# Performance work log

Hardware: AMD Instinct MI355X
Metric: run time of the kernel (lower is better)

The kernel has to match this reference:

```python
import jax, jax.numpy as jnp
import numpy as np

LN_EPS = 1e-5

def _linear(x, w, b):
    return x @ w.T + b

def _layernorm(x, g, b):
    mu = jnp.mean(x, axis=-1, keepdims=True)
    var = jnp.var(x, axis=-1, keepdims=True)
    return (x - mu) * jax.lax.rsqrt(var + LN_EPS) * g + b

def _depthwise_conv1d(x, w):
    # x: [B, S, D], w: [D, 1, 3] (torch layout), padding=1, groups=D, no bias
    xc = jnp.swapaxes(x, 1, 2)  # [B, D, S]
    y = jax.lax.conv_general_dilated(
        xc, w, window_strides=(1,), padding=[(1, 1)],
        dimension_numbers=('NCH', 'OIH', 'NCH'),
        feature_group_count=w.shape[0])
    return jnp.swapaxes(y, 1, 2)

def _ssm(x, A, B, C):
    # h_t = h_{t-1} A^T + x_t B^T ; y_t = h_t C^T
    bsz = x.shape[0]
    h0 = jnp.zeros((bsz, A.shape[0]), dtype=x.dtype)
    def step(h, xt):  # xt: [B, D]
        h = h @ A.T + xt @ B.T
        return h, h @ C.T
    _, ys = jax.lax.scan(step, h0, jnp.swapaxes(x, 0, 1))  # [S, B, D]
    return jnp.swapaxes(ys, 0, 1)

def setup_inputs() -> dict:
    key = jax.random.key(0)
    d_model, d_state, expand = 1024, 64, 2
    B, S = 4, 2048
    ks = jax.random.split(key, 16)
    sm = 1.0 / np.sqrt(d_model)
    inp = {
        'x': jax.random.normal(ks[0], (B, S, d_model), jnp.float32),
        'w1_w': jax.random.normal(ks[1], (d_model, d_model), jnp.float32) * sm,
        'w1_b': jnp.zeros((d_model,), jnp.float32),
        'v1_w': jax.random.normal(ks[2], (d_model, d_model), jnp.float32) * sm,
        'v1_b': jnp.zeros((d_model,), jnp.float32),
        'w2_w': jax.random.normal(ks[3], (d_model, d_model), jnp.float32) * sm,
        'w2_b': jnp.zeros((d_model,), jnp.float32),
        'conv_w': jax.random.normal(ks[4], (d_model, 1, 3), jnp.float32) * (1.0 / np.sqrt(3.0)),
        'A': jax.random.normal(ks[5], (d_state, d_state), jnp.float32) * 0.05,  # spectral radius ~0.4, stable scan
        'Bm': jax.random.normal(ks[6], (d_state, d_model), jnp.float32) * sm,
        'Cm': jax.random.normal(ks[7], (d_model, d_state), jnp.float32) * (1.0 / np.sqrt(d_state)),
        'ln1_g': jnp.ones((d_model,), jnp.float32),
        'ln1_b': jnp.zeros((d_model,), jnp.float32),
        'ln2_g': jnp.ones((d_model,), jnp.float32),
        'ln2_b': jnp.zeros((d_model,), jnp.float32),
        'ff1_w': jax.random.normal(ks[8], (expand * d_model, d_model), jnp.float32) * sm,
        'ff1_b': jnp.zeros((expand * d_model,), jnp.float32),
        'ff2_w': jax.random.normal(ks[9], (d_model, expand * d_model), jnp.float32) * (1.0 / np.sqrt(expand * d_model)),
        'ff2_b': jnp.zeros((d_model,), jnp.float32),
    }
    return inp

def reference(x, w1_w, w1_b, v1_w, v1_b, w2_w, w2_b, conv_w, A, Bm, Cm,
              ln1_g, ln1_b, ln2_g, ln2_b, ff1_w, ff1_b, ff2_w, ff2_b):
    residual = x
    h = _layernorm(x, ln1_g, ln1_b)
    # Mamba block
    x1 = _linear(h, w1_w, w1_b)
    xc = jax.nn.silu(_depthwise_conv1d(x1, conv_w))
    x_ssm = _ssm(xc, A, Bm, Cm)
    v = jax.nn.silu(_linear(h, v1_w, v1_b))
    h = _linear(x_ssm * v, w2_w, w2_b)
    x = h + residual
    residual = x
    h = _layernorm(x, ln2_g, ln2_b)
    h = _linear(jax.nn.gelu(_linear(h, ff1_w, ff1_b), approximate=False), ff2_w, ff2_b)
    return h + residual
```

## Files before the change

### kernel.cpp

```cpp
#include <hip/hip_runtime.h>
#include <hip/hip_bf16.h>

typedef unsigned short u16;
typedef __bf16 bf16x8 __attribute__((ext_vector_type(8)));
typedef float f32x4 __attribute__((ext_vector_type(4)));

#define DEV __device__ __forceinline__

DEV u16 f2bf(float f) {
  __hip_bfloat16 h = __float2bfloat16(f);
  union { __hip_bfloat16 h; u16 u; } c; c.h = h; return c.u;
}
DEV float bf2f(u16 u) {
  unsigned int x = ((unsigned int)u) << 16; float f;
  __builtin_memcpy(&f, &x, 4); return f;
}
DEV float silu_f(float x) { return x / (1.f + __expf(-x)); }
DEV float gelu_f(float x) { return 0.5f * x * (1.f + erff(x * 0.70710678118654752f)); }

DEV void gl_lds16(const void* g, void* l) {
  __builtin_amdgcn_global_load_lds(
      (const __attribute__((address_space(1))) void*)g,
      (__attribute__((address_space(3))) void*)l, 16, 0, 0);
}

template<int N> DEV void vmwait() {
  static_assert(N == 0 || N == 2 || N == 4, "unsupported vmcnt");
  if constexpr (N == 0)      asm volatile("s_waitcnt vmcnt(0)" ::: "memory");
  else if constexpr (N == 2) asm volatile("s_waitcnt vmcnt(2)" ::: "memory");
  else                       asm volatile("s_waitcnt vmcnt(4)" ::: "memory");
}

template<int BM, int EPI>
__global__ __launch_bounds__(512, 2)
void gemm256(const u16* __restrict__ A, const u16* __restrict__ Bw,
             const float* __restrict__ bias, const float* __restrict__ bias2,
             const float* __restrict__ resp,
             void* __restrict__ outp, void* __restrict__ outp2,
             int M, int N, int K)
{
  constexpr int WROWS = BM / 2;
  constexpr int MR = WROWS / 16;
  constexpr int NR = 4;
  constexpr int LA = BM / 64;
  constexpr int LB = 4;
  constexpr int AE = BM * 64;
  constexpr int BUFE = AE + 16384;
  __shared__ alignas(16) u16 lds[2 * BUFE];

  const int t = threadIdx.x;
  const int w = t >> 6, l = t & 63;
  const int wm = w >> 2, wn = w & 3;
  const int lr = l & 15, lq = l >> 4;

  const int nwg = gridDim.x;
  int lin = blockIdx.x;
  if ((nwg & 7) == 0) lin = (lin & 7) * (nwg >> 3) + (lin >> 3);
  const int nbx = N >> 8;
  const int by = lin / nbx, bx = lin - by * nbx;
  const int brow = by * BM, bcol = bx << 8;

  const int ir = l >> 3, ik = l & 7;
  const int kkl = ik ^ ir;
  const u16* gsA[LA];
  const u16* gsB[LB];
#pragma unroll
  for (int s = 0; s < LA; ++s)
    gsA[s] = A + (size_t)(brow + (w * LA + s) * 8 + ir) * K + kkl * 8;
#pragma unroll
  for (int s = 0; s < LB; ++s)
    gsB[s] = Bw + (size_t)(bcol + (w * LB + s) * 8 + ir) * K + kkl * 8;

  auto stageA = [&](int buf) {
#pragma unroll
    for (int s = 0; s < LA; ++s) {
      gl_lds16(gsA[s], &lds[buf * BUFE + (w * LA + s) * 512]);
      gsA[s] += 64;
    }
  };
  auto stageB = [&](int buf) {
#pragma unroll
    for (int s = 0; s < LB; ++s) {
      gl_lds16(gsB[s], &lds[buf * BUFE + AE + (w * LB + s) * 512]);
      gsB[s] += 64;
    }
  };

  f32x4 acc[MR][NR] = {};

  auto kstep = [&](int buf, int ks) {
    bf16x8 af[MR], bfr[NR];
#pragma unroll
    for (int mi = 0; mi < MR; ++mi) {
      const int ro = wm * WROWS + mi * 16 + lr;
      const int ck = (ks * 4 + lq) ^ (ro & 7);
      af[mi] = *(const bf16x8*)&lds[buf * BUFE + ro * 64 + ck * 8];
    }
#pragma unroll
    for (int ni = 0; ni < NR; ++ni) {
      const int ro = wn * 64 + ni * 16 + lr;
      const int ck = (ks * 4 + lq) ^ (ro & 7);
      bfr[ni] = *(const bf16x8*)&lds[buf * BUFE + AE + ro * 64 + ck * 8];
    }
    __builtin_amdgcn_s_setprio(1);
#pragma unroll
    for (int mi = 0; mi < MR; ++mi)
#pragma unroll
      for (int ni = 0; ni < NR; ++ni)
        acc[mi][ni] = __builtin_amdgcn_mfma_f32_16x16x32_bf16(af[mi], bfr[ni], acc[mi][ni], 0, 0, 0);
    __builtin_amdgcn_s_setprio(0);
  };

  stageA(0); stageB(0);
  const int nt = K >> 6;
  int cur = 0;
  for (int kt = 0; kt < nt; ++kt) {
    const int nxt = cur ^ 1;
    if (kt + 1 < nt) { stageA(nxt); vmwait<LA>(); }
    else             { vmwait<0>(); }
    __builtin_amdgcn_s_barrier();
    kstep(cur, 0);
    if (kt + 1 < nt) stageB(nxt);
    kstep(cur, 1);
    __builtin_amdgcn_s_barrier();
    cur = nxt;
  }

#pragma unroll
  for (int ni = 0; ni < NR; ++ni) {
    const int col = bcol + wn * 64 + ni * 16 + lr;
    float bv = 0.f;
    if (EPI == 3 || EPI == 4) bv = bias[col];
    if (EPI == 5) bv = (col < 1024) ? bias[col] : bias2[col - 1024];
#pragma unroll
    for (int mi = 0; mi < MR; ++mi) {
      const int row0 = brow + wm * WROWS + mi * 16 + lq * 4;
#pragma unroll
      for (int r = 0; r < 4; ++r) {
        const int row = row0 + r;
        const float raw = acc[mi][ni][r];
        if (EPI == 3) {
          const size_t idx = (size_t)row * N + col;
          ((float*)outp)[idx] = raw + bv + resp[idx];
        } else if (EPI == 4) {
          ((u16*)outp)[(size_t)row * N + col] = f2bf(gelu_f(raw + bv));
        } else {
          if (col < 1024) ((u16*)outp)[(size_t)row * 1024 + col] = f2bf(raw + bv);
          else ((u16*)outp2)[(size_t)row * 1024 + (col - 1024)] = f2bf(silu_f(raw + bv));
        }
      }
    }
  }
}

template<int EPI>
__global__ __launch_bounds__(256)
void gemm_bt(const u16* __restrict__ A, const u16* __restrict__ Bw,
             const float* __restrict__ bias, const u16* __restrict__ mulp,
             void* __restrict__ outp, int M, int N, int K)
{
  __shared__ u16 As[2][128 * 32];
  __shared__ u16 Bs[2][128 * 32];
  const int t = threadIdx.x;
  const int w = t >> 6, l = t & 63;
  const int wr = w >> 1, wc = w & 1;
  const int brow = blockIdx.y << 7;
  const int bcol = blockIdx.x << 7;

  const u16* gA0 = A + (size_t)(brow + (t >> 2)) * K + ((t & 3) << 3);
  const u16* gA1 = gA0 + (size_t)64 * K;
  int bn0 = bcol + (t >> 2);      if (bn0 > N - 1) bn0 = N - 1;
  int bn1 = bcol + 64 + (t >> 2); if (bn1 > N - 1) bn1 = N - 1;
  const u16* gB0 = Bw + (size_t)bn0 * K + ((t & 3) << 3);
  const u16* gB1 = Bw + (size_t)bn1 * K + ((t & 3) << 3);
  const int woff = w << 9;

  auto stage = [&](int b) {
    gl_lds16(gA0, &As[b][woff]);        gl_lds16(gA1, &As[b][2048 + woff]);
    gl_lds16(gB0, &Bs[b][woff]);        gl_lds16(gB1, &Bs[b][2048 + woff]);
    gA0 += 32; gA1 += 32; gB0 += 32; gB1 += 32;
  };

  f32x4 acc[4][4] = {};
  const int lr = l & 15, lk = (l >> 4) << 3;
  const int nt = K >> 5;

  stage(0);
  __syncthreads();
  int cur = 0;
  for (int kt = 0; kt < nt; ++kt) {
    if (kt + 1 < nt) stage(cur ^ 1);
    bf16x8 af[4], bfr[4];
#pragma unroll
    for (int i = 0; i < 4; ++i)
      af[i] = *(const bf16x8*)&As[cur][(wr * 64 + i * 16 + lr) * 32 + lk];
#pragma unroll
    for (int j = 0; j < 4; ++j)
      bfr[j] = *(const bf16x8*)&Bs[cur][(wc * 64 + j * 16 + lr) * 32 + lk];
    __builtin_amdgcn_s_setprio(1);
#pragma unroll
    for (int i = 0; i < 4; ++i)
#pragma unroll
      for (int j = 0; j < 4; ++j)
        acc[i][j] = __builtin_amdgcn_mfma_f32_16x16x32_bf16(af[i], bfr[j], acc[i][j], 0, 0, 0);
    __builtin_amdgcn_s_setprio(0);
    __syncthreads();
    cur ^= 1;
  }

  const int lq = l >> 4;
#pragma unroll
  for (int j = 0; j < 4; ++j) {
    const int col = bcol + wc * 64 + j * 16 + lr;
    if (col >= N) continue;
    const float bv = (EPI == 0 && bias) ? bias[col] : 0.f;
#pragma unroll
    for (int i = 0; i < 4; ++i) {
      const int row0 = brow + wr * 64 + i * 16 + lq * 4;
#pragma unroll
      for (int r = 0; r < 4; ++r) {
        const size_t idx = (size_t)(row0 + r) * N + col;
        const float raw = acc[i][j][r];
        if (EPI == 0) ((float*)outp)[idx] = raw + bv;
        else          ((u16*)outp)[idx]   = f2bf(raw * bf2f(mulp[idx]));
      }
    }
  }
}

__global__ __launch_bounds__(256)
void ln_bf16(const float* __restrict__ x, const float* __restrict__ g,
             const float* __restrict__ b, u16* __restrict__ out)
{
  const int row = blockIdx.x;
  const int t = threadIdx.x;
  const float4 v = ((const float4*)(x + (size_t)row * 1024))[t];
  float s = v.x + v.y + v.z + v.w;
  float sq = v.x * v.x + v.y * v.y + v.z * v.z + v.w * v.w;
#pragma unroll
  for (int o = 32; o; o >>= 1) { s += __shfl_xor(s, o); sq += __shfl_xor(sq, o); }
  __shared__ float ls[8];
  const int w = t >> 6, l = t & 63;
  if (l == 0) { ls[w] = s; ls[4 + w] = sq; }
  __syncthreads();
  s = ls[0] + ls[1] + ls[2] + ls[3];
  sq = ls[4] + ls[5] + ls[6] + ls[7];
  const float mean = s * (1.f / 1024.f);
  const float var = sq * (1.f / 1024.f) - mean * mean;
  const float rs = rsqrtf(var + 1e-5f);
  const float4 gg = ((const float4*)g)[t];
  const float4 bb = ((const float4*)b)[t];
  ushort4 o;
  o.x = f2bf((v.x - mean) * rs * gg.x + bb.x);
  o.y = f2bf((v.y - mean) * rs * gg.y + bb.y);
  o.z = f2bf((v.z - mean) * rs * gg.z + bb.z);
  o.w = f2bf((v.w - mean) * rs * gg.w + bb.w);
  ((ushort4*)(out + (size_t)row * 1024))[t] = o;
}

__global__ __launch_bounds__(256)
void conv_silu(const u16* __restrict__ x1, const float* __restrict__ cwT,
               u16* __restrict__ xc, int S)
{
  const size_t gid = (size_t)blockIdx.x * 256 + threadIdx.x;
  const int dq = (int)(gid & 255);
  const size_t tok = gid >> 8;
  const int s = (int)(tok % (size_t)S);
  ushort4 zz; zz.x = 0; zz.y = 0; zz.z = 0; zz.w = 0;
  const ushort4* base = (const ushort4*)x1 + tok * 256;
  const ushort4 xm = (s > 0) ? base[dq - 256] : zz;
  const ushort4 x0 = base[dq];
  const ushort4 xp = (s < S - 1) ? base[dq + 256] : zz;
  const float4 w0 = ((const float4*)cwT)[dq];
  const float4 w1 = ((const float4*)(cwT + 1024))[dq];
  const float4 w2 = ((const float4*)(cwT + 2048))[dq];
  ushort4 o;
  o.x = f2bf(silu_f(w0.x * bf2f(xm.x) + w1.x * bf2f(x0.x) + w2.x * bf2f(xp.x)));
  o.y = f2bf(silu_f(w0.y * bf2f(xm.y) + w1.y * bf2f(x0.y) + w2.y * bf2f(xp.y)));
  o.z = f2bf(silu_f(w0.z * bf2f(xm.z) + w1.z * bf2f(x0.z) + w2.z * bf2f(xp.z)));
  o.w = f2bf(silu_f(w0.w * bf2f(xm.w) + w1.w * bf2f(x0.w) + w2.w * bf2f(xp.w)));
  ((ushort4*)xc)[gid] = o;
}

__global__ __launch_bounds__(64)
void ssm_scan(const float* __restrict__ Amat, const float* __restrict__ U,
              u16* __restrict__ H, int S)
{
  const int b = blockIdx.y;
  const int c = blockIdx.x;
  const int j = threadIdx.x;
  const int s0 = c * 32;
  const int tstart = (s0 >= 32) ? (s0 - 32) : 0;
  float4 Ar[16];
#pragma unroll
  for (int q = 0; q < 16; ++q) Ar[q] = ((const float4*)(Amat + j * 64))[q];
  __shared__ float hb[64];
  float h = 0.f;
  const float* Ub = U + (size_t)b * S * 64;
  u16* Hb = H + (size_t)b * S * 64;
  for (int t = tstart; t < s0 + 32; ++t) {
    hb[j] = h;
    __syncthreads();
    float acc0 = Ub[(size_t)t * 64 + j];
#pragma unroll
    for (int q = 0; q < 16; ++q) {
      const float4 hv = *(const float4*)&hb[q * 4];
      acc0 += Ar[q].x * hv.x + Ar[q].y * hv.y + Ar[q].z * hv.z + Ar[q].w * hv.w;
    }
    __syncthreads();
    h = acc0;
    if (t >= s0) Hb[(size_t)t * 64 + j] = f2bf(h);
  }
}

__global__ __launch_bounds__(256)
void cvt_bf16(const float* __restrict__ in, u16* __restrict__ out, int n4)
{
  const int i = blockIdx.x * 256 + threadIdx.x;
  if (i < n4) {
    const float4 v = ((const float4*)in)[i];
    ushort4 o;
    o.x = f2bf(v.x); o.y = f2bf(v.y); o.z = f2bf(v.z); o.w = f2bf(v.w);
    ((ushort4*)out)[i] = o;
  }
}

__global__ __launch_bounds__(256)
void cvt_convw(const float* __restrict__ cw, float* __restrict__ cwT)
{
  const int d = blockIdx.x * 256 + threadIdx.x;
  if (d < 1024) {
    cwT[d]        = cw[d * 3 + 0];
    cwT[1024 + d] = cw[d * 3 + 1];
    cwT[2048 + d] = cw[d * 3 + 2];
  }
}

extern "C" void kernel_launch(void* const* d_in, const int* in_sizes, int n_in,
                              void* d_out, int out_size, void* d_ws, size_t ws_size,
                              hipStream_t stream)
{
  (void)in_sizes; (void)n_in; (void)out_size; (void)ws_size;
  const float* x     = (const float*)d_in[0];
  const float* w1_w  = (const float*)d_in[1];
  const float* w1_b  = (const float*)d_in[2];
  const float* v1_w  = (const float*)d_in[3];
  const float* v1_b  = (const float*)d_in[4];
  const float* w2_w  = (const float*)d_in[5];
  const float* w2_b  = (const float*)d_in[6];
  const float* convw = (const float*)d_in[7];
  const float* Amat  = (const float*)d_in[8];
  const float* Bm    = (const float*)d_in[9];
  const float* Cm    = (const float*)d_in[10];
  const float* ln1_g = (const float*)d_in[11];
  const float* ln1_b = (const float*)d_in[12];
  const float* ln2_g = (const float*)d_in[13];
  const float* ln2_b = (const float*)d_in[14];
  const float* ff1_w = (const float*)d_in[15];
  const float* ff1_b = (const float*)d_in[16];
  const float* ff2_w = (const float*)d_in[17];
  const float* ff2_b = (const float*)d_in[18];

  const int S = 2048, D = 1024, Dff = 2048, NS = 64, BATCH = 4;
  const int NT = BATCH * S;

  char* ws = (char*)d_ws;
  size_t off = 0;
  auto alc = [&](size_t bytes) -> void* {
    void* p = ws + off; off += (bytes + 255) & ~(size_t)255; return p;
  };
  u16*   wb1  = (u16*)alc((size_t)D * D * 2);
  u16*   wv1  = (u16*)alc((size_t)D * D * 2);
  u16*   ww2  = (u16*)alc((size_t)D * D * 2);
  u16*   wf1  = (u16*)alc((size_t)Dff * D * 2);
  u16*   wf2  = (u16*)alc((size_t)D * Dff * 2);
  u16*   wBm  = (u16*)alc((size_t)NS * D * 2);
  u16*   wCm  = (u16*)alc((size_t)D * NS * 2);
  float* cwT  = (float*)alc((size_t)3 * D * 4);
  u16*   h1g  = (u16*)alc((size_t)NT * D * 2);
  u16*   vbuf = (u16*)alc((size_t)NT * D * 2);
  float* Xb   = (float*)alc((size_t)NT * D * 4);
  u16*   xch2 = (u16*)alc((size_t)NT * D * 2);
  float* Ubuf = (float*)alc((size_t)NT * NS * 4);
  u16*   Hbuf = (u16*)alc((size_t)NT * NS * 2);
  u16*   f1b  = (u16*)alc((size_t)NT * Dff * 2);
  u16*   x1b  = (u16*)Xb;

  const dim3 blk(256);
  auto cvt = [&](const float* src, u16* dst, int n) {
    const int n4 = n / 4;
    hipLaunchKernelGGL(cvt_bf16, dim3((n4 + 255) / 256), blk, 0, stream, src, dst, n4);
  };
  cvt(w1_w, wb1, D * D);
  cvt(v1_w, wv1, D * D);
  cvt(w2_w, ww2, D * D);
  cvt(ff1_w, wf1, Dff * D);
  cvt(ff2_w, wf2, D * Dff);
  cvt(Bm, wBm, NS * D);
  cvt(Cm, wCm, D * NS);
  hipLaunchKernelGGL(cvt_convw, dim3(4), blk, 0, stream, convw, cwT);

  hipLaunchKernelGGL(ln_bf16, dim3(NT), blk, 0, stream, x, ln1_g, ln1_b, h1g);
  hipLaunchKernelGGL((gemm256<256, 5>), dim3(256), dim3(512), 0, stream,
                     h1g, wb1, w1_b, v1_b, (const float*)nullptr,
                     (void*)x1b, (void*)vbuf, NT, 2 * D, D);
  hipLaunchKernelGGL(conv_silu, dim3(NT), blk, 0, stream, x1b, cwT, xch2, S);
  hipLaunchKernelGGL((gemm_bt<0>), dim3(1, NT / 128), blk, 0, stream,
                     xch2, wBm, (const float*)nullptr, (const u16*)nullptr,
                     (void*)Ubuf, NT, NS, D);
  hipLaunchKernelGGL(ssm_scan, dim3(S / 32, BATCH), dim3(64), 0, stream,
                     Amat, Ubuf, Hbuf, S);
  hipLaunchKernelGGL((gemm_bt<2>), dim3(D / 128, NT / 128), blk, 0, stream,
                     Hbuf, wCm, (const float*)nullptr, vbuf,
                     (void*)h1g, NT, D, NS);
  hipLaunchKernelGGL((gemm256<128, 3>), dim3(256), dim3(512), 0, stream,
                     h1g, ww2, w2_b, (const float*)nullptr, x,
                     (void*)Xb, (void*)nullptr, NT, D, D);
  hipLaunchKernelGGL(ln_bf16, dim3(NT), blk, 0, stream, Xb, ln2_g, ln2_b, xch2);
  hipLaunchKernelGGL((gemm256<256, 4>), dim3(256), dim3(512), 0, stream,
                     xch2, wf1, ff1_b, (const float*)nullptr, (const float*)nullptr,
                     (void*)f1b, (void*)nullptr, NT, Dff, D);
  hipLaunchKernelGGL((gemm256<128, 3>), dim3(256), dim3(512), 0, stream,
                     f1b, wf2, ff2_b, (const float*)nullptr, Xb,
                     d_out, (void*)nullptr, NT, D, Dff);
}
```

Measured before the change: 302.3 us.

## Replace 256-wide double-buffered GEMM with single-buffer 128x128 tiles and fuse weight casts

Replaces the 512-thread double-buffered 256-wide GEMM with a 256-thread 128x128 tile kernel. The new kernel uses a single LDS buffer with sync-load-compute and targets 3 blocks per CU, launching more, smaller blocks. It also merges the seven weight-conversion launches into one kernel and drops the setprio hints in the small GEMM. The trade is more workgroups and occupancy against losing explicit load/compute overlap inside a block and reusing less data per tile.

```diff
diff --git a/kernel.cpp b/kernel.cpp
--- a/kernel.cpp
+++ b/kernel.cpp
@@ -24,117 +24,78 @@
       (__attribute__((address_space(3))) void*)l, 16, 0, 0);
 }
 
-template<int N> DEV void vmwait() {
-  static_assert(N == 0 || N == 2 || N == 4, "unsupported vmcnt");
-  if constexpr (N == 0)      asm volatile("s_waitcnt vmcnt(0)" ::: "memory");
-  else if constexpr (N == 2) asm volatile("s_waitcnt vmcnt(2)" ::: "memory");
-  else                       asm volatile("s_waitcnt vmcnt(4)" ::: "memory");
-}
-
-template<int BM, int EPI>
-__global__ __launch_bounds__(512, 2)
-void gemm256(const u16* __restrict__ A, const u16* __restrict__ Bw,
+template<int EPI>
+__global__ __launch_bounds__(256, 3)
+void gemm128(const u16* __restrict__ A, const u16* __restrict__ Bw,
              const float* __restrict__ bias, const float* __restrict__ bias2,
              const float* __restrict__ resp,
              void* __restrict__ outp, void* __restrict__ outp2,
              int M, int N, int K)
 {
-  constexpr int WROWS = BM / 2;
-  constexpr int MR = WROWS / 16;
-  constexpr int NR = 4;
-  constexpr int LA = BM / 64;
-  constexpr int LB = 4;
-  constexpr int AE = BM * 64;
-  constexpr int BUFE = AE + 16384;
-  __shared__ alignas(16) u16 lds[2 * BUFE];
+  __shared__ alignas(16) u16 As[128 * 64];
+  __shared__ alignas(16) u16 Bs[128 * 64];
 
   const int t = threadIdx.x;
   const int w = t >> 6, l = t & 63;
-  const int wm = w >> 2, wn = w & 3;
+  const int wm = w >> 1, wn = w & 1;
   const int lr = l & 15, lq = l >> 4;
+  const int ir = l >> 3, ik = l & 7;
+  const int kkl = ik ^ ir;
 
   const int nwg = gridDim.x;
   int lin = blockIdx.x;
-  if ((nwg & 7) == 0) lin = (lin & 7) * (nwg >> 3) + (lin >> 3);
-  const int nbx = N >> 8;
+  lin = (lin & 7) * (nwg >> 3) + (lin >> 3);
+  const int nbx = N >> 7;
   const int by = lin / nbx, bx = lin - by * nbx;
-  const int brow = by * BM, bcol = bx << 8;
-
-  const int ir = l >> 3, ik = l & 7;
-  const int kkl = ik ^ ir;
-  const u16* gsA[LA];
-  const u16* gsB[LB];
-#pragma unroll
-  for (int s = 0; s < LA; ++s)
-    gsA[s] = A + (size_t)(brow + (w * LA + s) * 8 + ir) * K + kkl * 8;
-#pragma unroll
-  for (int s = 0; s < LB; ++s)
-    gsB[s] = Bw + (size_t)(bcol + (w * LB + s) * 8 + ir) * K + kkl * 8;
-
-  auto stageA = [&](int buf) {
-#pragma unroll
-    for (int s = 0; s < LA; ++s) {
-      gl_lds16(gsA[s], &lds[buf * BUFE + (w * LA + s) * 512]);
-      gsA[s] += 64;
-    }
-  };
-  auto stageB = [&](int buf) {
-#pragma unroll
-    for (int s = 0; s < LB; ++s) {
-      gl_lds16(gsB[s], &lds[buf * BUFE + AE + (w * LB + s) * 512]);
-      gsB[s] += 64;
-    }
-  };
-
-  f32x4 acc[MR][NR] = {};
-
-  auto kstep = [&](int buf, int ks) {
-    bf16x8 af[MR], bfr[NR];
-#pragma unroll
-    for (int mi = 0; mi < MR; ++mi) {
-      const int ro = wm * WROWS + mi * 16 + lr;
-      const int ck = (ks * 4 + lq) ^ (ro & 7);
-      af[mi] = *(const bf16x8*)&lds[buf * BUFE + ro * 64 + ck * 8];
-    }
-#pragma unroll
-    for (int ni = 0; ni < NR; ++ni) {
-      const int ro = wn * 64 + ni * 16 + lr;
-      const int ck = (ks * 4 + lq) ^ (ro & 7);
-      bfr[ni] = *(const bf16x8*)&lds[buf * BUFE + AE + ro * 64 + ck * 8];
-    }
-    __builtin_amdgcn_s_setprio(1);
-#pragma unroll
-    for (int mi = 0; mi < MR; ++mi)
-#pragma unroll
-      for (int ni = 0; ni < NR; ++ni)
-        acc[mi][ni] = __builtin_amdgcn_mfma_f32_16x16x32_bf16(af[mi], bfr[ni], acc[mi][ni], 0, 0, 0);
-    __builtin_amdgcn_s_setprio(0);
-  };
-
-  stageA(0); stageB(0);
+  const int brow = by << 7, bcol = bx << 7;
+
+  const u16* gA = A + (size_t)(brow + w * 8 + ir) * K + kkl * 8;
+  const u16* gB = Bw + (size_t)(bcol + w * 8 + ir) * K + kkl * 8;
+
+  f32x4 acc[4][4] = {};
   const int nt = K >> 6;
-  int cur = 0;
+
   for (int kt = 0; kt < nt; ++kt) {
-    const int nxt = cur ^ 1;
-    if (kt + 1 < nt) { stageA(nxt); vmwait<LA>(); }
-    else             { vmwait<0>(); }
-    __builtin_amdgcn_s_barrier();
-    kstep(cur, 0);
-    if (kt + 1 < nt) stageB(nxt);
-    kstep(cur, 1);
-    __builtin_amdgcn_s_barrier();
-    cur = nxt;
-  }
-
-#pragma unroll
-  for (int ni = 0; ni < NR; ++ni) {
+#pragma unroll
+    for (int s = 0; s < 4; ++s) {
+      gl_lds16(gA + (size_t)(s * 32) * K, &As[(s * 32 + w * 8) * 64]);
+      gl_lds16(gB + (size_t)(s * 32) * K, &Bs[(s * 32 + w * 8) * 64]);
+    }
+    gA += 64; gB += 64;
+    __syncthreads();
+#pragma unroll
+    for (int ks = 0; ks < 2; ++ks) {
+      bf16x8 af[4], bf[4];
+#pragma unroll
+      for (int mi = 0; mi < 4; ++mi) {
+        const int ro = wm * 64 + mi * 16 + lr;
+        const int ck = (ks * 4 + lq) ^ (ro & 7);
+        af[mi] = *(const bf16x8*)&As[ro * 64 + ck * 8];
+      }
+#pragma unroll
+      for (int ni = 0; ni < 4; ++ni) {
+        const int ro = wn * 64 + ni * 16 + lr;
+        const int ck = (ks * 4 + lq) ^ (ro & 7);
+        bf[ni] = *(const bf16x8*)&Bs[ro * 64 + ck * 8];
+      }
+#pragma unroll
+      for (int mi = 0; mi < 4; ++mi)
+#pragma unroll
+        for (int ni = 0; ni < 4; ++ni)
+          acc[mi][ni] = __builtin_amdgcn_mfma_f32_16x16x32_bf16(af[mi], bf[ni], acc[mi][ni], 0, 0, 0);
+    }
+    __syncthreads();
+  }
+
+#pragma unroll
+  for (int ni = 0; ni < 4; ++ni) {
     const int col = bcol + wn * 64 + ni * 16 + lr;
     float bv = 0.f;
     if (EPI == 3 || EPI == 4) bv = bias[col];
     if (EPI == 5) bv = (col < 1024) ? bias[col] : bias2[col - 1024];
 #pragma unroll
-    for (int mi = 0; mi < MR; ++mi) {
-      const int row0 = brow + wm * WROWS + mi * 16 + lq * 4;
+    for (int mi = 0; mi < 4; ++mi) {
+      const int row0 = brow + wm * 64 + mi * 16 + lq * 4;
 #pragma unroll
       for (int r = 0; r < 4; ++r) {
         const int row = row0 + r;
@@ -197,13 +158,11 @@
 #pragma unroll
     for (int j = 0; j < 4; ++j)
       bfr[j] = *(const bf16x8*)&Bs[cur][(wc * 64 + j * 16 + lr) * 32 + lk];
-    __builtin_amdgcn_s_setprio(1);
 #pragma unroll
     for (int i = 0; i < 4; ++i)
 #pragma unroll
       for (int j = 0; j < 4; ++j)
         acc[i][j] = __builtin_amdgcn_mfma_f32_16x16x32_bf16(af[i], bfr[j], acc[i][j], 0, 0, 0);
-    __builtin_amdgcn_s_setprio(0);
     __syncthreads();
     cur ^= 1;
   }
@@ -313,16 +272,23 @@
   }
 }
 
-__global__ __launch_bounds__(256)
-void cvt_bf16(const float* __restrict__ in, u16* __restrict__ out, int n4)
-{
-  const int i = blockIdx.x * 256 + threadIdx.x;
-  if (i < n4) {
-    const float4 v = ((const float4*)in)[i];
-    ushort4 o;
-    o.x = f2bf(v.x); o.y = f2bf(v.y); o.z = f2bf(v.z); o.w = f2bf(v.w);
-    ((ushort4*)out)[i] = o;
-  }
+struct CvtArgs {
+  const float* src[7];
+  unsigned beg4[8];
+};
+
+__global__ __launch_bounds__(256)
+void cvt_all(CvtArgs a, u16* __restrict__ dst)
+{
+  const unsigned i = blockIdx.x * 256 + threadIdx.x;
+  if (i >= a.beg4[7]) return;
+  int s = 0;
+#pragma unroll
+  for (int k = 1; k < 7; ++k) if (i >= a.beg4[k]) s = k;
+  const float4 v = ((const float4*)a.src[s])[i - a.beg4[s]];
+  ushort4 o;
+  o.x = f2bf(v.x); o.y = f2bf(v.y); o.z = f2bf(v.z); o.w = f2bf(v.w);
+  ((ushort4*)dst)[i] = o;
 }
 
 __global__ __launch_bounds__(256)
@@ -387,21 +353,25 @@
   u16*   x1b  = (u16*)Xb;
 
   const dim3 blk(256);
-  auto cvt = [&](const float* src, u16* dst, int n) {
-    const int n4 = n / 4;
-    hipLaunchKernelGGL(cvt_bf16, dim3((n4 + 255) / 256), blk, 0, stream, src, dst, n4);
-  };
-  cvt(w1_w, wb1, D * D);
-  cvt(v1_w, wv1, D * D);
-  cvt(w2_w, ww2, D * D);
-  cvt(ff1_w, wf1, Dff * D);
-  cvt(ff2_w, wf2, D * Dff);
-  cvt(Bm, wBm, NS * D);
-  cvt(Cm, wCm, D * NS);
+
+  {
+    CvtArgs a;
+    const unsigned q = (unsigned)(D * D / 4);
+    const unsigned qf = (unsigned)(Dff * D / 4);
+    const unsigned qs = (unsigned)(NS * D / 4);
+    a.src[0] = w1_w;  a.src[1] = v1_w;  a.src[2] = w2_w;
+    a.src[3] = ff1_w; a.src[4] = ff2_w; a.src[5] = Bm; a.src[6] = Cm;
+    a.beg4[0] = 0;
+    a.beg4[1] = q;          a.beg4[2] = 2 * q;      a.beg4[3] = 3 * q;
+    a.beg4[4] = 3 * q + qf; a.beg4[5] = 3 * q + 2 * qf;
+    a.beg4[6] = 3 * q + 2 * qf + qs;
+    a.beg4[7] = 3 * q + 2 * qf + 2 * qs;
+    hipLaunchKernelGGL(cvt_all, dim3((a.beg4[7] + 255) / 256), blk, 0, stream, a, wb1);
+  }
   hipLaunchKernelGGL(cvt_convw, dim3(4), blk, 0, stream, convw, cwT);
 
   hipLaunchKernelGGL(ln_bf16, dim3(NT), blk, 0, stream, x, ln1_g, ln1_b, h1g);
-  hipLaunchKernelGGL((gemm256<256, 5>), dim3(256), dim3(512), 0, stream,
+  hipLaunchKernelGGL((gemm128<5>), dim3((NT / 128) * (2 * D / 128)), blk, 0, stream,
                      h1g, wb1, w1_b, v1_b, (const float*)nullptr,
                      (void*)x1b, (void*)vbuf, NT, 2 * D, D);
   hipLaunchKernelGGL(conv_silu, dim3(NT), blk, 0, stream, x1b, cwT, xch2, S);
@@ -413,14 +383,14 @@
   hipLaunchKernelGGL((gemm_bt<2>), dim3(D / 128, NT / 128), blk, 0, stream,
                      Hbuf, wCm, (const float*)nullptr, vbuf,
                      (void*)h1g, NT, D, NS);
-  hipLaunchKernelGGL((gemm256<128, 3>), dim3(256), dim3(512), 0, stream,
+  hipLaunchKernelGGL((gemm128<3>), dim3((NT / 128) * (D / 128)), blk, 0, stream,
                      h1g, ww2, w2_b, (const float*)nullptr, x,
                      (void*)Xb, (void*)nullptr, NT, D, D);
   hipLaunchKernelGGL(ln_bf16, dim3(NT), blk, 0, stream, Xb, ln2_g, ln2_b, xch2);
-  hipLaunchKernelGGL((gemm256<256, 4>), dim3(256), dim3(512), 0, stream,
+  hipLaunchKernelGGL((gemm128<4>), dim3((NT / 128) * (Dff / 128)), blk, 0, stream,
                      xch2, wf1, ff1_b, (const float*)nullptr, (const float*)nullptr,
                      (void*)f1b, (void*)nullptr, NT, Dff, D);
-  hipLaunchKernelGGL((gemm256<128, 3>), dim3(256), dim3(512), 0, stream,
+  hipLaunchKernelGGL((gemm128<3>), dim3((NT / 128) * (D / 128)), blk, 0, stream,
                      f1b, wf2, ff2_b, (const float*)nullptr, Xb,
                      d_out, (void*)nullptr, NT, D, Dff);
 }
```

Result: slower. 319.2 us (+5.6%).
